# Optimization experiments

Measured on AMD Instinct MI355X. Metric: run time of the kernel, lower is better.

## Reference

```python
import jax, jax.numpy as jnp
import numpy as np

D_MODEL = 4096
D_LATENT = 512
NUM_HEADS = 32
HEAD_DIM = D_MODEL // NUM_HEADS  # 128
ROPE_THETA = 10000.0
BATCH, SEQ = 2, 2048


def _rotate_half(x):
    x1, x2 = jnp.split(x, 2, axis=-1)
    return jnp.concatenate([-x2, x1], axis=-1)


def _rope_cos_sin(positions, head_dim, theta, dtype):
    # positions: [B, S] -> cos/sin: [B, S, 1, head_dim]
    inv_freq = 1.0 / (theta ** (jnp.arange(0, head_dim, 2, dtype=jnp.float32) / head_dim))
    freqs = positions.astype(jnp.float32)[..., None] * inv_freq  # [B,S,hd/2]
    emb = jnp.concatenate([freqs, freqs], axis=-1)               # [B,S,hd]
    return jnp.cos(emb)[:, :, None, :].astype(dtype), jnp.sin(emb)[:, :, None, :].astype(dtype)


def setup_inputs() -> dict:
    key = jax.random.key(0)
    ks = jax.random.split(key, 6)
    s = 0.02
    return {
        "hidden_states": jax.random.normal(ks[0], (BATCH, SEQ, D_MODEL), jnp.float32),
        "Wq": jax.random.normal(ks[1], (D_MODEL, NUM_HEADS * HEAD_DIM), jnp.float32) * s,
        "Wc": jax.random.normal(ks[2], (D_MODEL, D_LATENT), jnp.float32) * s,
        "Wk": jax.random.normal(ks[3], (D_LATENT, NUM_HEADS * HEAD_DIM), jnp.float32) * s,
        "Wv": jax.random.normal(ks[4], (D_LATENT, NUM_HEADS * HEAD_DIM), jnp.float32) * s,
        "Wo": jax.random.normal(ks[5], (NUM_HEADS * HEAD_DIM, D_MODEL), jnp.float32) * s,
    }


def reference(hidden_states, Wq, Wc, Wk, Wv, Wo):
    B, S, _ = hidden_states.shape
    H, Dh = NUM_HEADS, HEAD_DIM

    q = (hidden_states @ Wq).reshape(B, S, H, Dh)
    kv_latent = hidden_states @ Wc                     # [B,S,d_latent]
    k = (kv_latent @ Wk).reshape(B, S, H, Dh)
    v = (kv_latent @ Wv).reshape(B, S, H, Dh)

    # RoPE: q uses positions [0..S), k uses positions [0..S) (no past cache)
    pos = jnp.broadcast_to(jnp.arange(S)[None, :], (B, S))
    cos, sin = _rope_cos_sin(pos, Dh, ROPE_THETA, q.dtype)
    q = q * cos + _rotate_half(q) * sin
    k = k * cos + _rotate_half(k) * sin

    # standard attention, no mask (faithful to attention_mask=None path)
    scale = 1.0 / np.sqrt(Dh)
    scores = jnp.einsum("bqhd,bkhd->bhqk", q, k) * scale
    probs = jax.nn.softmax(scores, axis=-1)
    attn = jnp.einsum("bhqk,bkhd->bqhd", probs, v)     # [B,S,H,Dh]

    out = attn.reshape(B, S, H * Dh) @ Wo
    return out
```

## Files before the change

### kernel.cpp

```cpp
#include <hip/hip_runtime.h>
#include <hip/hip_bf16.h>
#include <cstdint>
#include <cstddef>

#define D_MODEL 4096
#define D_LATENT 512
#define NUM_HEADS 32
#define HEAD_DIM 128
#define BATCH 2
#define SEQ 2048
#define ROWS (BATCH*SEQ)

typedef __attribute__((ext_vector_type(8))) short bf16x8;
typedef __attribute__((ext_vector_type(4))) float f32x4;
typedef __attribute__((ext_vector_type(16))) float f32x16;
typedef unsigned int uint;

static __device__ __forceinline__ unsigned short f2bf(float f){
  union { float f; uint32_t u; } v; v.f = f;
  uint32_t r = (v.u + 0x7fffu + ((v.u >> 16) & 1u)) >> 16;
  return (unsigned short)r;
}
static __device__ __forceinline__ float bf2f(unsigned short h){
  union { uint32_t u; float f; } v; v.u = ((uint32_t)h) << 16;
  return v.f;
}
static __device__ __forceinline__ uint cvtpk(float lo, float hi2){
  uint r;
  asm("v_cvt_pk_bf16_f32 %0, %1, %2" : "=v"(r) : "v"(lo), "v"(hi2));
  return r;
}
static __device__ __forceinline__ void gload16(const void* g, void* l){
  __builtin_amdgcn_global_load_lds(
      (const __attribute__((address_space(1))) void*)g,
      (__attribute__((address_space(3))) void*)l, 16, 0, 0);
}

__global__ __launch_bounds__(256) void f32_to_bf16(
    const float* __restrict__ in, unsigned short* __restrict__ out){
  const size_t i = ((size_t)blockIdx.x * 256 + threadIdx.x) * 8;
  const float4 lo = *(const float4*)(in + i);
  const float4 hi = *(const float4*)(in + i + 4);
  uint4 d; unsigned short* dp = (unsigned short*)&d;
  dp[0]=f2bf(lo.x); dp[1]=f2bf(lo.y); dp[2]=f2bf(lo.z); dp[3]=f2bf(lo.w);
  dp[4]=f2bf(hi.x); dp[5]=f2bf(hi.y); dp[6]=f2bf(hi.z); dp[7]=f2bf(hi.w);
  *(uint4*)(out + i) = d;
}

__global__ __launch_bounds__(256) void transpose_convert(
    const float* __restrict__ W, unsigned short* __restrict__ Wt, int K, int N){
  __shared__ float tile[64][65];
  const int k0 = blockIdx.x * 64, n0 = blockIdx.y * 64;
  const int t = threadIdx.x;
  #pragma unroll
  for (int j = 0; j < 16; ++j){
    const int idx = t + 256*j;
    const int r = idx >> 6, c = idx & 63;
    tile[r][c] = W[(size_t)(k0 + r) * N + n0 + c];
  }
  __syncthreads();
  #pragma unroll
  for (int j = 0; j < 16; ++j){
    const int idx = t + 256*j;
    const int r = idx >> 6, c = idx & 63;
    Wt[(size_t)(n0 + r) * K + k0 + c] = f2bf(tile[c][r]);
  }
}

__global__ __launch_bounds__(256) void v_transpose(
    const unsigned short* __restrict__ v, unsigned short* __restrict__ vt){
  __shared__ unsigned short tile[64][72];
  const int s0 = blockIdx.x * 64, d0 = blockIdx.y * 64, bh = blockIdx.z;
  const int b = bh >> 5, h = bh & 31;
  const int t = threadIdx.x;
  #pragma unroll
  for (int j = 0; j < 2; ++j){
    const int idx = t + 256*j;
    const int r = idx >> 3, ch = idx & 7;
    *(uint4*)&tile[r][ch*8] =
      *(const uint4*)&v[(size_t)(b*SEQ + s0 + r) * D_MODEL + h*128 + d0 + ch*8];
  }
  __syncthreads();
  #pragma unroll
  for (int j = 0; j < 16; ++j){
    const int idx = t + 256*j;
    const int r = idx >> 6, c = idx & 63;
    vt[((size_t)bh*128 + d0 + r) * SEQ + s0 + c] = tile[c][r];
  }
}

__global__ __launch_bounds__(256) void rope_table_kernel(float* __restrict__ ct,
                                                         float* __restrict__ st){
  const int i = blockIdx.x * 256 + threadIdx.x;
  if (i >= SEQ * 64) return;
  const int s = i >> 6, j = i & 63;
  const float inv = powf(10000.0f, -(float)j / 64.0f);
  const double a = (double)s * (double)inv;
  ct[i] = (float)cos(a);
  st[i] = (float)sin(a);
}

__global__ __launch_bounds__(256) void rope_apply(unsigned short* __restrict__ buf,
    const float* __restrict__ ct, const float* __restrict__ st, float scale){
  const int i = blockIdx.x * 256 + threadIdx.x;
  const int j = i & 63;
  const int tmp = i >> 6;
  const int h = tmp & 31;
  const int row = tmp >> 5;
  const int s = row & (SEQ - 1);
  const float c = ct[s*64 + j], sn = st[s*64 + j];
  const size_t base = (size_t)row * D_MODEL + (size_t)h * 128;
  const float x1 = bf2f(buf[base + j]);
  const float x2 = bf2f(buf[base + j + 64]);
  buf[base + j]      = f2bf((x1 * c - x2 * sn) * scale);
  buf[base + j + 64] = f2bf((x2 * c + x1 * sn) * scale);
}

template<bool OF32>
__global__ __launch_bounds__(256) void gemm_kernel(
    const unsigned short* __restrict__ A, const unsigned short* __restrict__ Bt,
    void* __restrict__ Cp, int M, int N, int K){
  __shared__ __align__(16) char As[128 * 128];
  __shared__ __align__(16) char Bs[128 * 128];
  const int t = threadIdx.x;
  const int m0 = blockIdx.y * 128, n0 = blockIdx.x * 128;
  const int l = t & 63, wid = t >> 6;
  const int wr = wid >> 1, wcn = wid & 1;
  const int lr = l & 15, lg = l >> 4;

  const int srow = l >> 3;
  const int gch  = (l & 7) ^ srow;
  const unsigned short* gA = A  + (size_t)(m0 + wid*32 + srow) * K + gch*8;
  const unsigned short* gB = Bt + (size_t)(n0 + wid*32 + srow) * K + gch*8;
  char* lA = As + wid*4096;
  char* lB = Bs + wid*4096;

  f32x4 acc[4][4];
  #pragma unroll
  for (int i = 0; i < 4; ++i)
    #pragma unroll
    for (int j = 0; j < 4; ++j)
      #pragma unroll
      for (int r = 0; r < 4; ++r) acc[i][j][r] = 0.0f;

  const int kTiles = K >> 6;
  for (int kt = 0; kt < kTiles; ++kt){
    const size_t ko = (size_t)kt << 6;
    #pragma unroll
    for (int i = 0; i < 4; ++i){
      gload16(gA + (size_t)i*8*K + ko, lA + i*1024);
      gload16(gB + (size_t)i*8*K + ko, lB + i*1024);
    }
    __syncthreads();
    #pragma unroll
    for (int kc = 0; kc < 2; ++kc){
      bf16x8 af[4], bfv[4];
      const int ch = kc*4 + lg;
      #pragma unroll
      for (int mb = 0; mb < 4; ++mb){
        const int row = wr*64 + mb*16 + lr;
        af[mb] = *(const bf16x8*)(As + row*128 + ((ch ^ (row & 7)) * 16));
      }
      #pragma unroll
      for (int nb = 0; nb < 4; ++nb){
        const int row = wcn*64 + nb*16 + lr;
        bfv[nb] = *(const bf16x8*)(Bs + row*128 + ((ch ^ (row & 7)) * 16));
      }
      #pragma unroll
      for (int mb = 0; mb < 4; ++mb)
        #pragma unroll
        for (int nb = 0; nb < 4; ++nb)
          acc[mb][nb] = __builtin_amdgcn_mfma_f32_16x16x32_bf16(af[mb], bfv[nb], acc[mb][nb], 0, 0, 0);
    }
    __syncthreads();
  }
  #pragma unroll
  for (int mb = 0; mb < 4; ++mb)
    #pragma unroll
    for (int nb = 0; nb < 4; ++nb)
      #pragma unroll
      for (int r = 0; r < 4; ++r){
        const int row = m0 + wr*64 + mb*16 + lg*4 + r;
        const int col = n0 + wcn*64 + nb*16 + lr;
        if constexpr (OF32) ((float*)Cp)[(size_t)row * N + col] = acc[mb][nb][r];
        else ((unsigned short*)Cp)[(size_t)row * N + col] = f2bf(acc[mb][nb][r]);
      }
}

template<int MH>
static __device__ __forceinline__ void rdAh(bf16x8 (&a_)[4][2], const char* buf,
                                            int wr, int lr, int lg){
  #pragma unroll
  for (int mm = 0; mm < 4; ++mm)
    #pragma unroll
    for (int kc = 0; kc < 2; ++kc){
      const int row = wr*128 + (MH*4 + mm)*16 + lr;
      const int ch = kc*4 + lg;
      a_[mm][kc] = *(const bf16x8*)(buf + row*128 + ((ch ^ (row & 7)) * 16));
    }
}
template<int NH>
static __device__ __forceinline__ void rdBh(bf16x8 (&b_)[2][2][2], const char* buf,
                                            int wc, int lr, int lg){
  #pragma unroll
  for (int nn = 0; nn < 2; ++nn)
    #pragma unroll
    for (int kc = 0; kc < 2; ++kc){
      const int row = wc*64 + (NH*2 + nn)*16 + lr;
      const int ch = kc*4 + lg;
      b_[NH][nn][kc] = *(const bf16x8*)(buf + row*128 + ((ch ^ (row & 7)) * 16));
    }
}
template<int MH, int NH>
static __device__ __forceinline__ void mfq(f32x4 (&acc)[8][4],
    const bf16x8 (&a_)[4][2], const bf16x8 (&b_)[2][2][2]){
  __builtin_amdgcn_s_setprio(1);
  #pragma unroll
  for (int kc = 0; kc < 2; ++kc)
    #pragma unroll
    for (int mm = 0; mm < 4; ++mm)
      #pragma unroll
      for (int nn = 0; nn < 2; ++nn)
        acc[MH*4+mm][NH*2+nn] = __builtin_amdgcn_mfma_f32_16x16x32_bf16(
            a_[mm][kc], b_[NH][nn][kc], acc[MH*4+mm][NH*2+nn], 0, 0, 0);
  __builtin_amdgcn_s_setprio(0);
}

#define G256_BAR  __builtin_amdgcn_s_barrier()
#define G256_LGK0 do{ asm volatile("s_waitcnt lgkmcnt(0)" ::: "memory"); \
                      __builtin_amdgcn_sched_barrier(0); }while(0)
#define G256_VM(n) asm volatile("s_waitcnt vmcnt(" #n ")" ::: "memory")

template<bool OF32>
__global__ __launch_bounds__(512, 2) void gemm256_kernel(
    const unsigned short* __restrict__ A, const unsigned short* __restrict__ Bt,
    void* __restrict__ Cp, int M, int N, int K){
  __shared__ __align__(16) char lds[131072];
  char* const As0 = lds;
  char* const As1 = lds + 32768;
  char* const Bs0 = lds + 65536;
  char* const Bs1 = lds + 98304;

  const int t = threadIdx.x;
  const int l = t & 63, wid = t >> 6;
  const int wr = wid >> 2, wc = wid & 3;
  const int lr = l & 15, lg = l >> 4;
  const int m0 = blockIdx.y * 256, n0 = blockIdx.x * 256;

  const int srow = t >> 3;
  const int pch = t & 7;
  const int gch = pch ^ (srow & 7);
  const unsigned short* gAb = A  + (size_t)(m0 + srow) * K + gch*8;
  const unsigned short* gBb = Bt + (size_t)(n0 + srow) * K + gch*8;
  const int ldso = srow*128 + pch*16;

  auto stA = [&](char* dst, int half, int kcol){
    const unsigned short* g = gAb + (size_t)half*128*K + kcol;
    gload16(g,                dst + half*16384 + ldso);
    gload16(g + (size_t)64*K, dst + half*16384 + 8192 + ldso);
  };
  auto stB = [&](char* dst, int half, int kcol){
    const unsigned short* g = gBb + (size_t)half*128*K + kcol;
    gload16(g,                dst + half*16384 + ldso);
    gload16(g + (size_t)64*K, dst + half*16384 + 8192 + ldso);
  };

  f32x4 acc[8][4];
  #pragma unroll
  for (int m = 0; m < 8; ++m)
    #pragma unroll
    for (int n = 0; n < 4; ++n)
      #pragma unroll
      for (int r = 0; r < 4; ++r) acc[m][n][r] = 0.0f;
  bf16x8 a_[4][2];
  bf16x8 b_[2][2][2];

  const int niter = K >> 7;
  stA(As0, 0, 0); stA(As0, 1, 0); stB(Bs0, 0, 0); stB(Bs0, 1, 0);
  stA(As1, 0, 64);
  G256_VM(2);
  G256_BAR;
  __builtin_amdgcn_sched_barrier(0);

  for (int j = 0; j < niter; ++j){
    const int k0 = j << 7;
    const bool more = (j + 1 < niter);
    rdAh<0>(a_, As0, wr, lr, lg);
    rdBh<0>(b_, Bs0, wc, lr, lg);
    stA(As1, 1, k0 + 64);
    G256_BAR; G256_LGK0;
    mfq<0,0>(acc, a_, b_);
    G256_BAR;
    rdBh<1>(b_, Bs0, wc, lr, lg);
    stB(Bs1, 0, k0 + 64);
    G256_BAR; G256_LGK0;
    mfq<0,1>(acc, a_, b_);
    G256_BAR;
    rdAh<1>(a_, As0, wr, lr, lg);
    stB(Bs1, 1, k0 + 64);
    G256_BAR; G256_LGK0;
    mfq<1,0>(acc, a_, b_);
    G256_BAR;
    if (more){ stA(As0, 0, k0 + 128); G256_VM(2); }
    else     { G256_VM(0); }
    G256_BAR;
    __builtin_amdgcn_sched_barrier(0);
    mfq<1,1>(acc, a_, b_);
    G256_BAR;
    rdAh<0>(a_, As1, wr, lr, lg);
    rdBh<0>(b_, Bs1, wc, lr, lg);
    if (more) stA(As0, 1, k0 + 128);
    G256_BAR; G256_LGK0;
    mfq<0,0>(acc, a_, b_);
    G256_BAR;
    rdBh<1>(b_, Bs1, wc, lr, lg);
    if (more) stB(Bs0, 0, k0 + 128);
    G256_BAR; G256_LGK0;
    mfq<0,1>(acc, a_, b_);
    G256_BAR;
    rdAh<1>(a_, As1, wr, lr, lg);
    if (more) stB(Bs0, 1, k0 + 128);
    G256_BAR; G256_LGK0;
    mfq<1,0>(acc, a_, b_);
    G256_BAR;
    if (more){ stA(As1, 0, k0 + 192); G256_VM(2); }
    G256_BAR;
    __builtin_amdgcn_sched_barrier(0);
    mfq<1,1>(acc, a_, b_);
    G256_BAR;
  }

  #pragma unroll
  for (int m = 0; m < 8; ++m)
    #pragma unroll
    for (int n = 0; n < 4; ++n)
      #pragma unroll
      for (int r = 0; r < 4; ++r){
        const int row = m0 + wr*128 + m*16 + lg*4 + r;
        const int col = n0 + wc*64 + n*16 + lr;
        if constexpr (OF32) ((float*)Cp)[(size_t)row * N + col] = acc[m][n][r];
        else ((unsigned short*)Cp)[(size_t)row * N + col] = f2bf(acc[m][n][r]);
      }
}

__global__ __launch_bounds__(512) void attn_kernel(
    const unsigned short* __restrict__ q, const unsigned short* __restrict__ kp,
    const unsigned short* __restrict__ vt, unsigned short* __restrict__ o){
  __shared__ __align__(16) char Ks[2 * 16384];
  __shared__ __align__(16) char Vs[2 * 16384];
  const int t = threadIdx.x;
  const int l = t & 63, w = t >> 6;
  const int lq = l & 31, hi = l >> 5;
  const int bh = blockIdx.x, qb = blockIdx.y;
  const int b = bh >> 5;
  const size_t qbase = (size_t)b * SEQ + qb*256 + w*32;
  const size_t cb = (size_t)(bh & 31) * 128;

  auto stageKV = [&](int buf, int kb){
    const size_t kr0 = (size_t)b * SEQ + (size_t)kb*64;
    char* kdst = Ks + buf*16384 + w*2048;
    char* vdst = Vs + buf*16384 + w*2048;
    #pragma unroll
    for (int i = 0; i < 2; ++i){
      const int r = w*8 + i*4 + (l >> 4);
      const int g = (l & 15) ^ (r & 7);
      gload16(kp + (kr0 + r) * D_MODEL + cb + g*8, kdst + i*1024);
    }
    #pragma unroll
    for (int i = 0; i < 2; ++i){
      const int r = w*16 + i*8 + (l >> 3);
      const int g = (l & 7) ^ (r & 7);
      gload16(vt + ((size_t)bh*128 + r) * SEQ + (size_t)kb*64 + g*8, vdst + i*1024);
    }
  };

  bf16x8 qf[8];
  #pragma unroll
  for (int dc = 0; dc < 8; ++dc)
    qf[dc] = *(const bf16x8*)(q + (qbase + lq) * D_MODEL + cb + dc*16 + hi*8);

  f32x16 O[4];
  #pragma unroll
  for (int nb = 0; nb < 4; ++nb)
    #pragma unroll
    for (int r = 0; r < 16; ++r) O[nb][r] = 0.0f;
  float m = -1e30f, lsum = 0.0f;

  stageKV(0, 0);
  int cur = 0;
  for (int kb = 0; kb < SEQ/64; ++kb){
    const bool more = (kb + 1 < SEQ/64);
    if (more){
      stageKV(cur ^ 1, kb + 1);
      asm volatile("s_waitcnt vmcnt(4)" ::: "memory");
    } else {
      asm volatile("s_waitcnt vmcnt(0)" ::: "memory");
    }
    __builtin_amdgcn_s_barrier();
    __builtin_amdgcn_sched_barrier(0);
    const char* Kb = Ks + cur*16384;
    const char* Vb = Vs + cur*16384;

    f32x16 s0, s1;
    #pragma unroll
    for (int r = 0; r < 16; ++r){ s0[r] = 0.0f; s1[r] = 0.0f; }
    __builtin_amdgcn_s_setprio(1);
    #pragma unroll
    for (int dc = 0; dc < 8; ++dc){
      const int ch = dc*2 + hi;
      const bf16x8 k0 = *(const bf16x8*)(Kb + lq*256 + ((ch ^ (lq & 7)) * 16));
      const bf16x8 k1 = *(const bf16x8*)(Kb + (32 + lq)*256 + ((ch ^ (lq & 7)) * 16));
      s0 = __builtin_amdgcn_mfma_f32_32x32x16_bf16(k0, qf[dc], s0, 0, 0, 0);
      s1 = __builtin_amdgcn_mfma_f32_32x32x16_bf16(k1, qf[dc], s1, 0, 0, 0);
    }
    __builtin_amdgcn_s_setprio(0);

    float mt = s0[0];
    #pragma unroll
    for (int r = 1; r < 16; ++r) mt = fmaxf(mt, s0[r]);
    #pragma unroll
    for (int r = 0; r < 16; ++r) mt = fmaxf(mt, s1[r]);
    mt = fmaxf(mt, __shfl_xor(mt, 32));

    if (!__all(mt <= m + 8.0f)){
      const float mnew = fmaxf(m, mt);
      const float al = __builtin_amdgcn_exp2f(m - mnew);
      m = mnew;
      lsum *= al;
      float alb[16];
      #pragma unroll
      for (int r = 0; r < 16; ++r){
        const int crow = (r & 3) + 8*(r >> 2) + 4*hi;
        alb[r] = __shfl(al, crow);
      }
      #pragma unroll
      for (int nb = 0; nb < 4; ++nb)
        #pragma unroll
        for (int r = 0; r < 16; ++r) O[nb][r] *= alb[r];
    }

    float E[32];
    float sum = 0.0f;
    #pragma unroll
    for (int r = 0; r < 16; ++r){ E[r] = __builtin_amdgcn_exp2f(s0[r] - m); sum += E[r]; }
    #pragma unroll
    for (int r = 0; r < 16; ++r){ E[16 + r] = __builtin_amdgcn_exp2f(s1[r] - m); sum += E[16 + r]; }
    sum += __shfl_xor(sum, 32);
    lsum += sum;

    bf16x8 pa[4];
    #pragma unroll
    for (int c = 0; c < 4; ++c){
      const int rb = c * 8;
      const uint a_ = cvtpk(E[rb + 0], E[rb + 1]);
      const uint b_ = cvtpk(E[rb + 2], E[rb + 3]);
      const uint c_ = cvtpk(E[rb + 4], E[rb + 5]);
      const uint d_ = cvtpk(E[rb + 6], E[rb + 7]);
      const uint sa = (uint)__shfl_xor((int)a_, 32);
      const uint sb = (uint)__shfl_xor((int)b_, 32);
      const uint sc = (uint)__shfl_xor((int)c_, 32);
      const uint sd = (uint)__shfl_xor((int)d_, 32);
      union { uint u[4]; bf16x8 v; } uu;
      uu.u[0] = hi ? sc : a_;
      uu.u[1] = hi ? sd : b_;
      uu.u[2] = hi ? c_ : sa;
      uu.u[3] = hi ? d_ : sb;
      pa[c] = uu.v;
    }

    __builtin_amdgcn_s_setprio(1);
    #pragma unroll
    for (int c = 0; c < 4; ++c){
      const int ch = c*2 + hi;
      #pragma unroll
      for (int nb = 0; nb < 4; ++nb){
        const int vr = nb*32 + lq;
        const bf16x8 vf = *(const bf16x8*)(Vb + vr*128 + ((ch ^ (vr & 7)) * 16));
        O[nb] = __builtin_amdgcn_mfma_f32_32x32x16_bf16(pa[c], vf, O[nb], 0, 0, 0);
      }
    }
    __builtin_amdgcn_s_setprio(0);
    __builtin_amdgcn_s_barrier();
    __builtin_amdgcn_sched_barrier(0);
    cur ^= 1;
  }

  const float rinv = 1.0f / lsum;
  float rb_[16];
  #pragma unroll
  for (int r = 0; r < 16; ++r){
    const int crow = (r & 3) + 8*(r >> 2) + 4*hi;
    rb_[r] = __shfl(rinv, crow);
  }
  #pragma unroll
  for (int nb = 0; nb < 4; ++nb)
    #pragma unroll
    for (int r = 0; r < 16; ++r){
      const int crow = (r & 3) + 8*(r >> 2) + 4*hi;
      o[(qbase + crow) * D_MODEL + cb + nb*32 + lq] = f2bf(O[nb][r] * rb_[r]);
    }
}

extern "C" void kernel_launch(void* const* d_in, const int* in_sizes, int n_in,
                              void* d_out, int out_size, void* d_ws, size_t ws_size,
                              hipStream_t stream){
  const float* hidden = (const float*)d_in[0];
  const float* Wq = (const float*)d_in[1];
  const float* Wc = (const float*)d_in[2];
  const float* Wk = (const float*)d_in[3];
  const float* Wv = (const float*)d_in[4];
  const float* Wo = (const float*)d_in[5];
  float* out = (float*)d_out;

  char* ws = (char*)d_ws;
  size_t off = 0;
  auto alloc = [&](size_t bytes)->char*{
    char* p = ws + off; off += (bytes + 255) & ~(size_t)255; return p;
  };
  unsigned short* Wqt  = (unsigned short*)alloc((size_t)D_MODEL * D_MODEL * 2);
  unsigned short* Wct  = (unsigned short*)alloc((size_t)D_LATENT * D_MODEL * 2);
  unsigned short* Wkt  = (unsigned short*)alloc((size_t)D_MODEL * D_LATENT * 2);
  unsigned short* Wvt  = (unsigned short*)alloc((size_t)D_MODEL * D_LATENT * 2);
  unsigned short* Wot  = (unsigned short*)alloc((size_t)D_MODEL * D_MODEL * 2);
  unsigned short* latent = (unsigned short*)alloc((size_t)ROWS * D_LATENT * 2);
  unsigned short* qbuf = (unsigned short*)alloc((size_t)ROWS * D_MODEL * 2);
  unsigned short* kbuf = (unsigned short*)alloc((size_t)ROWS * D_MODEL * 2);
  unsigned short* vbuf = (unsigned short*)alloc((size_t)ROWS * D_MODEL * 2);
  unsigned short* attnb= (unsigned short*)alloc((size_t)ROWS * D_MODEL * 2);
  float* ctab = (float*)alloc((size_t)SEQ * 64 * 4);
  float* stab = (float*)alloc((size_t)SEQ * 64 * 4);
  unsigned short* hbf   = attnb;
  unsigned short* vtbuf = Wqt;

  const dim3 B256(256);
  const float qscale = 0.08838834764831845f * 1.4426950408889634f;

  f32_to_bf16<<<(ROWS*(size_t)D_MODEL)/2048, B256, 0, stream>>>(hidden, hbf);
  transpose_convert<<<dim3(64, 64), B256, 0, stream>>>(Wq, Wqt, D_MODEL, D_MODEL);
  transpose_convert<<<dim3(64, 8),  B256, 0, stream>>>(Wc, Wct, D_MODEL, D_LATENT);
  transpose_convert<<<dim3(8, 64),  B256, 0, stream>>>(Wk, Wkt, D_LATENT, D_MODEL);
  transpose_convert<<<dim3(8, 64),  B256, 0, stream>>>(Wv, Wvt, D_LATENT, D_MODEL);
  transpose_convert<<<dim3(64, 64), B256, 0, stream>>>(Wo, Wot, D_MODEL, D_MODEL);
  rope_table_kernel<<<512, B256, 0, stream>>>(ctab, stab);

  gemm_kernel<false><<<dim3(D_LATENT/128, ROWS/128), B256, 0, stream>>>(hbf, Wct, latent, ROWS, D_LATENT, D_MODEL);
  gemm256_kernel<false><<<dim3(D_MODEL/256, ROWS/256), dim3(512), 0, stream>>>(hbf,    Wqt, qbuf, ROWS, D_MODEL, D_MODEL);
  gemm256_kernel<false><<<dim3(D_MODEL/256, ROWS/256), dim3(512), 0, stream>>>(latent, Wkt, kbuf, ROWS, D_MODEL, D_LATENT);
  gemm256_kernel<false><<<dim3(D_MODEL/256, ROWS/256), dim3(512), 0, stream>>>(latent, Wvt, vbuf, ROWS, D_MODEL, D_LATENT);

  v_transpose<<<dim3(SEQ/64, HEAD_DIM/64, BATCH*NUM_HEADS), B256, 0, stream>>>(vbuf, vtbuf);

  rope_apply<<<(ROWS * NUM_HEADS * 64) / 256, B256, 0, stream>>>(qbuf, ctab, stab, qscale);
  rope_apply<<<(ROWS * NUM_HEADS * 64) / 256, B256, 0, stream>>>(kbuf, ctab, stab, 1.0f);

  attn_kernel<<<dim3(BATCH * NUM_HEADS, SEQ/256), dim3(512), 0, stream>>>(qbuf, kbuf, vtbuf, attnb);

  gemm256_kernel<true><<<dim3(D_MODEL/256, ROWS/256), dim3(512), 0, stream>>>(attnb, Wot, out, ROWS, D_MODEL, D_MODEL);
}
```

Before: 653.2 us.

## Software-pipeline PV with next QK in attention, fuse Q RoPE and K/V GEMMs

Result: slower. 754.7 us (+15.5%).

```diff
diff --git a/kernel.cpp b/kernel.cpp
--- a/kernel.cpp
+++ b/kernel.cpp
@@ -234,7 +234,8 @@
 template<bool OF32>
 __global__ __launch_bounds__(512, 2) void gemm256_kernel(
     const unsigned short* __restrict__ A, const unsigned short* __restrict__ Bt,
-    void* __restrict__ Cp, int M, int N, int K){
+    void* __restrict__ Cp, void* __restrict__ Cp2, int nsplit, int ldc,
+    int M, int N, int K){
   __shared__ __align__(16) char lds[131072];
   char* const As0 = lds;
   char* const As1 = lds + 32768;
@@ -330,6 +331,9 @@
     G256_BAR;
   }
 
+  void* outp = Cp;
+  int c0 = n0;
+  if (n0 >= nsplit){ outp = Cp2; c0 = n0 - nsplit; }
   #pragma unroll
   for (int m = 0; m < 8; ++m)
     #pragma unroll
@@ -337,15 +341,16 @@
       #pragma unroll
       for (int r = 0; r < 4; ++r){
         const int row = m0 + wr*128 + m*16 + lg*4 + r;
-        const int col = n0 + wc*64 + n*16 + lr;
-        if constexpr (OF32) ((float*)Cp)[(size_t)row * N + col] = acc[m][n][r];
-        else ((unsigned short*)Cp)[(size_t)row * N + col] = f2bf(acc[m][n][r]);
-      }
-}
-
-__global__ __launch_bounds__(512) void attn_kernel(
+        const int col = c0 + wc*64 + n*16 + lr;
+        if constexpr (OF32) ((float*)outp)[(size_t)row * ldc + col] = acc[m][n][r];
+        else ((unsigned short*)outp)[(size_t)row * ldc + col] = f2bf(acc[m][n][r]);
+      }
+}
+
+__global__ __launch_bounds__(512, 4) void attn_kernel(
     const unsigned short* __restrict__ q, const unsigned short* __restrict__ kp,
-    const unsigned short* __restrict__ vt, unsigned short* __restrict__ o){
+    const unsigned short* __restrict__ vt, const float* __restrict__ ct,
+    const float* __restrict__ st, unsigned short* __restrict__ o){
   __shared__ __align__(16) char Ks[2 * 16384];
   __shared__ __align__(16) char Vs[2 * 16384];
   const int t = threadIdx.x;
@@ -356,16 +361,18 @@
   const size_t qbase = (size_t)b * SEQ + qb*256 + w*32;
   const size_t cb = (size_t)(bh & 31) * 128;
 
-  auto stageKV = [&](int buf, int kb){
+  auto stageK = [&](int buf, int kb){
     const size_t kr0 = (size_t)b * SEQ + (size_t)kb*64;
     char* kdst = Ks + buf*16384 + w*2048;
-    char* vdst = Vs + buf*16384 + w*2048;
     #pragma unroll
     for (int i = 0; i < 2; ++i){
       const int r = w*8 + i*4 + (l >> 4);
       const int g = (l & 15) ^ (r & 7);
       gload16(kp + (kr0 + r) * D_MODEL + cb + g*8, kdst + i*1024);
     }
+  };
+  auto stageV = [&](int buf, int kb){
+    char* vdst = Vs + buf*16384 + w*2048;
     #pragma unroll
     for (int i = 0; i < 2; ++i){
       const int r = w*16 + i*8 + (l >> 3);
@@ -378,6 +385,27 @@
   #pragma unroll
   for (int dc = 0; dc < 8; ++dc)
     qf[dc] = *(const bf16x8*)(q + (qbase + lq) * D_MODEL + cb + dc*16 + hi*8);
+  {
+    const float qsc = 0.08838834764831845f * 1.4426950408889634f;
+    const int s = qb*256 + w*32 + lq;
+    #pragma unroll
+    for (int dc = 0; dc < 4; ++dc){
+      const int j0 = dc*16 + hi*8;
+      const float4 c0 = *(const float4*)(ct + s*64 + j0);
+      const float4 c1 = *(const float4*)(ct + s*64 + j0 + 4);
+      const float4 s0_ = *(const float4*)(st + s*64 + j0);
+      const float4 s1_ = *(const float4*)(st + s*64 + j0 + 4);
+      const float cc[8] = {c0.x,c0.y,c0.z,c0.w,c1.x,c1.y,c1.z,c1.w};
+      const float ss[8] = {s0_.x,s0_.y,s0_.z,s0_.w,s1_.x,s1_.y,s1_.z,s1_.w};
+      #pragma unroll
+      for (int e = 0; e < 8; ++e){
+        const float x1 = bf2f((unsigned short)qf[dc][e]);
+        const float x2 = bf2f((unsigned short)qf[dc + 4][e]);
+        qf[dc][e]     = (short)f2bf((x1 * cc[e] - x2 * ss[e]) * qsc);
+        qf[dc + 4][e] = (short)f2bf((x2 * cc[e] + x1 * ss[e]) * qsc);
+      }
+    }
+  }
 
   f32x16 O[4];
   #pragma unroll
@@ -385,21 +413,21 @@
     #pragma unroll
     for (int r = 0; r < 16; ++r) O[nb][r] = 0.0f;
   float m = -1e30f, lsum = 0.0f;
-
-  stageKV(0, 0);
-  int cur = 0;
+  bf16x8 pa[4];
+
+  stageK(0, 0); stageV(0, 0);
+
   for (int kb = 0; kb < SEQ/64; ++kb){
     const bool more = (kb + 1 < SEQ/64);
     if (more){
-      stageKV(cur ^ 1, kb + 1);
+      stageK((kb + 1) & 1, kb + 1);
       asm volatile("s_waitcnt vmcnt(4)" ::: "memory");
     } else {
-      asm volatile("s_waitcnt vmcnt(0)" ::: "memory");
+      asm volatile("s_waitcnt vmcnt(2)" ::: "memory");
     }
     __builtin_amdgcn_s_barrier();
     __builtin_amdgcn_sched_barrier(0);
-    const char* Kb = Ks + cur*16384;
-    const char* Vb = Vs + cur*16384;
+    const char* Kb = Ks + (kb & 1)*16384;
 
     f32x16 s0, s1;
     #pragma unroll
@@ -413,7 +441,23 @@
       s0 = __builtin_amdgcn_mfma_f32_32x32x16_bf16(k0, qf[dc], s0, 0, 0, 0);
       s1 = __builtin_amdgcn_mfma_f32_32x32x16_bf16(k1, qf[dc], s1, 0, 0, 0);
     }
+    if (kb > 0){
+      const char* Vp = Vs + ((kb + 1) & 1)*16384;
+      #pragma unroll
+      for (int c = 0; c < 4; ++c){
+        const int ch = c*2 + hi;
+        #pragma unroll
+        for (int nb = 0; nb < 4; ++nb){
+          const int vr = nb*32 + lq;
+          const bf16x8 vf = *(const bf16x8*)(Vp + vr*128 + ((ch ^ (vr & 7)) * 16));
+          O[nb] = __builtin_amdgcn_mfma_f32_32x32x16_bf16(pa[c], vf, O[nb], 0, 0, 0);
+        }
+      }
+    }
     __builtin_amdgcn_s_setprio(0);
+    __builtin_amdgcn_s_barrier();
+    __builtin_amdgcn_sched_barrier(0);
+    if (more) stageV((kb + 1) & 1, kb + 1);
 
     float mt = s0[0];
     #pragma unroll
@@ -427,16 +471,13 @@
       const float al = __builtin_amdgcn_exp2f(m - mnew);
       m = mnew;
       lsum *= al;
-      float alb[16];
       #pragma unroll
       for (int r = 0; r < 16; ++r){
         const int crow = (r & 3) + 8*(r >> 2) + 4*hi;
-        alb[r] = __shfl(al, crow);
-      }
-      #pragma unroll
-      for (int nb = 0; nb < 4; ++nb)
+        const float albr = __shfl(al, crow);
         #pragma unroll
-        for (int r = 0; r < 16; ++r) O[nb][r] *= alb[r];
+        for (int nb = 0; nb < 4; ++nb) O[nb][r] *= albr;
+      }
     }
 
     float E[32];
@@ -448,7 +489,6 @@
     sum += __shfl_xor(sum, 32);
     lsum += sum;
 
-    bf16x8 pa[4];
     #pragma unroll
     for (int c = 0; c < 4; ++c){
       const int rb = c * 8;
@@ -467,38 +507,34 @@
       uu.u[3] = hi ? d_ : sb;
       pa[c] = uu.v;
     }
-
-    __builtin_amdgcn_s_setprio(1);
+  }
+
+  asm volatile("s_waitcnt vmcnt(0)" ::: "memory");
+  __builtin_amdgcn_s_barrier();
+  __builtin_amdgcn_sched_barrier(0);
+  {
+    const char* Vp = Vs + ((SEQ/64 - 1) & 1)*16384;
     #pragma unroll
     for (int c = 0; c < 4; ++c){
       const int ch = c*2 + hi;
       #pragma unroll
       for (int nb = 0; nb < 4; ++nb){
         const int vr = nb*32 + lq;
-        const bf16x8 vf = *(const bf16x8*)(Vb + vr*128 + ((ch ^ (vr & 7)) * 16));
+        const bf16x8 vf = *(const bf16x8*)(Vp + vr*128 + ((ch ^ (vr & 7)) * 16));
         O[nb] = __builtin_amdgcn_mfma_f32_32x32x16_bf16(pa[c], vf, O[nb], 0, 0, 0);
       }
     }
-    __builtin_amdgcn_s_setprio(0);
-    __builtin_amdgcn_s_barrier();
-    __builtin_amdgcn_sched_barrier(0);
-    cur ^= 1;
   }
 
   const float rinv = 1.0f / lsum;
-  float rb_[16];
   #pragma unroll
   for (int r = 0; r < 16; ++r){
     const int crow = (r & 3) + 8*(r >> 2) + 4*hi;
-    rb_[r] = __shfl(rinv, crow);
-  }
-  #pragma unroll
-  for (int nb = 0; nb < 4; ++nb)
-    #pragma unroll
-    for (int r = 0; r < 16; ++r){
-      const int crow = (r & 3) + 8*(r >> 2) + 4*hi;
-      o[(qbase + crow) * D_MODEL + cb + nb*32 + lq] = f2bf(O[nb][r] * rb_[r]);
-    }
+    const float rb_ = __shfl(rinv, crow);
+    #pragma unroll
+    for (int nb = 0; nb < 4; ++nb)
+      o[(qbase + crow) * D_MODEL + cb + nb*32 + lq] = f2bf(O[nb][r] * rb_);
+  }
 }
 
 extern "C" void kernel_launch(void* const* d_in, const int* in_sizes, int n_in,
@@ -519,8 +555,7 @@
   };
   unsigned short* Wqt  = (unsigned short*)alloc((size_t)D_MODEL * D_MODEL * 2);
   unsigned short* Wct  = (unsigned short*)alloc((size_t)D_LATENT * D_MODEL * 2);
-  unsigned short* Wkt  = (unsigned short*)alloc((size_t)D_MODEL * D_LATENT * 2);
-  unsigned short* Wvt  = (unsigned short*)alloc((size_t)D_MODEL * D_LATENT * 2);
+  unsigned short* Wkvt = (unsigned short*)alloc((size_t)2 * D_MODEL * D_LATENT * 2);
   unsigned short* Wot  = (unsigned short*)alloc((size_t)D_MODEL * D_MODEL * 2);
   unsigned short* latent = (unsigned short*)alloc((size_t)ROWS * D_LATENT * 2);
   unsigned short* qbuf = (unsigned short*)alloc((size_t)ROWS * D_MODEL * 2);
@@ -533,27 +568,28 @@
   unsigned short* vtbuf = Wqt;
 
   const dim3 B256(256);
-  const float qscale = 0.08838834764831845f * 1.4426950408889634f;
 
   f32_to_bf16<<<(ROWS*(size_t)D_MODEL)/2048, B256, 0, stream>>>(hidden, hbf);
   transpose_convert<<<dim3(64, 64), B256, 0, stream>>>(Wq, Wqt, D_MODEL, D_MODEL);
   transpose_convert<<<dim3(64, 8),  B256, 0, stream>>>(Wc, Wct, D_MODEL, D_LATENT);
-  transpose_convert<<<dim3(8, 64),  B256, 0, stream>>>(Wk, Wkt, D_LATENT, D_MODEL);
-  transpose_convert<<<dim3(8, 64),  B256, 0, stream>>>(Wv, Wvt, D_LATENT, D_MODEL);
+  transpose_convert<<<dim3(8, 64),  B256, 0, stream>>>(Wk, Wkvt, D_LATENT, D_MODEL);
+  transpose_convert<<<dim3(8, 64),  B256, 0, stream>>>(Wv, Wkvt + (size_t)D_MODEL*D_LATENT, D_LATENT, D_MODEL);
   transpose_convert<<<dim3(64, 64), B256, 0, stream>>>(Wo, Wot, D_MODEL, D_MODEL);
   rope_table_kernel<<<512, B256, 0, stream>>>(ctab, stab);
 
   gemm_kernel<false><<<dim3(D_LATENT/128, ROWS/128), B256, 0, stream>>>(hbf, Wct, latent, ROWS, D_LATENT, D_MODEL);
-  gemm256_kernel<false><<<dim3(D_MODEL/256, ROWS/256), dim3(512), 0, stream>>>(hbf,    Wqt, qbuf, ROWS, D_MODEL, D_MODEL);
-  gemm256_kernel<false><<<dim3(D_MODEL/256, ROWS/256), dim3(512), 0, stream>>>(latent, Wkt, kbuf, ROWS, D_MODEL, D_LATENT);
-  gemm256_kernel<false><<<dim3(D_MODEL/256, ROWS/256), dim3(512), 0, stream>>>(latent, Wvt, vbuf, ROWS, D_MODEL, D_LATENT);
+  gemm256_kernel<false><<<dim3(D_MODEL/256, ROWS/256), dim3(512), 0, stream>>>(
+      hbf, Wqt, qbuf, qbuf, 1 << 30, D_MODEL, ROWS, D_MODEL, D_MODEL);
+  gemm256_kernel<false><<<dim3(2*D_MODEL/256, ROWS/256), dim3(512), 0, stream>>>(
+      latent, Wkvt, kbuf, vbuf, D_MODEL, D_MODEL, ROWS, 2*D_MODEL, D_LATENT);
 
   v_transpose<<<dim3(SEQ/64, HEAD_DIM/64, BATCH*NUM_HEADS), B256, 0, stream>>>(vbuf, vtbuf);
 
-  rope_apply<<<(ROWS * NUM_HEADS * 64) / 256, B256, 0, stream>>>(qbuf, ctab, stab, qscale);
   rope_apply<<<(ROWS * NUM_HEADS * 64) / 256, B256, 0, stream>>>(kbuf, ctab, stab, 1.0f);
 
-  attn_kernel<<<dim3(BATCH * NUM_HEADS, SEQ/256), dim3(512), 0, stream>>>(qbuf, kbuf, vtbuf, attnb);
-
-  gemm256_kernel<true><<<dim3(D_MODEL/256, ROWS/256), dim3(512), 0, stream>>>(attnb, Wot, out, ROWS, D_MODEL, D_MODEL);
-}
+  attn_kernel<<<dim3(BATCH * NUM_HEADS, SEQ/256), dim3(512), 0, stream>>>(
+      qbuf, kbuf, vtbuf, ctab, stab, attnb);
+
+  gemm256_kernel<true><<<dim3(D_MODEL/256, ROWS/256), dim3(512), 0, stream>>>(
+      attnb, Wot, out, out, 1 << 30, D_MODEL, ROWS, D_MODEL, D_MODEL);
+}
```
